# Optimization experiments

Measured on AMD Instinct MI355X. Metric: run time of the kernel, lower is better.

Reference implementation:

```python
import jax, jax.numpy as jnp
import numpy as np

HEADS = 4


def rel_to_abs(x):
    """Convert relative logits [..., L, 2L-1] to absolute [..., L, L].
    out[..., i, j] = x[..., i, j - i + L - 1]."""
    L = x.shape[-2]
    idx = jnp.arange(L)[None, :] - jnp.arange(L)[:, None] + (L - 1)  # [L, L]
    idx = jnp.broadcast_to(idx, x.shape[:-1] + (L,))
    return jnp.take_along_axis(x, idx, axis=-1)


def setup_inputs() -> dict:
    key = jax.random.key(0)
    ks = jax.random.split(key, 5)
    b, c, h, w = 2, 256, 64, 64
    dh = c // HEADS
    return {
        "x": jax.random.normal(ks[0], (b, c, h, w), jnp.float32),
        "w_qkv": jax.random.normal(ks[1], (3 * c, c), jnp.float32) / np.float32(np.sqrt(c)),
        "w_out": jax.random.normal(ks[2], (c, c), jnp.float32) / np.float32(np.sqrt(c)),
        "rel_height": jax.random.normal(ks[3], (2 * h - 1, dh), jnp.float32),
        "rel_width": jax.random.normal(ks[4], (2 * w - 1, dh), jnp.float32),
    }


def reference(x, w_qkv, w_out, rel_height, rel_width):
    b, c, h, w = x.shape
    dh = c // HEADS
    N = h * w
    scale = dh ** -0.5

    # 1x1 conv == per-pixel matmul over channels
    qkv = jnp.einsum('bchw,oc->bohw', x, w_qkv)  # [b, 3c, h, w]
    q, k, v = jnp.split(qkv, 3, axis=1)

    def to_heads(t):  # [b, c, h, w] -> [b, H, N, dh]
        return t.reshape(b, HEADS, dh, N).transpose(0, 1, 3, 2)

    q = to_heads(q) * scale
    k = to_heads(k)
    v = to_heads(v)

    # content-content scores over spatial positions
    content = jnp.einsum('bnid,bnjd->bnij', q, k)  # [b, H, N, N]

    q5 = q.reshape(b, HEADS, h, w, dh)  # [b, H, x, y, dh]
    # width relative logits: [b,H,x,y,2w-1] -> abs -> [b,H,x,y,jw]
    rw = rel_to_abs(jnp.einsum('bnxyd,rd->bnxyr', q5, rel_width))
    # height relative logits on transposed spatial: [b,H,y,x,2h-1] -> [b,H,y,x,jh]
    rh = rel_to_abs(jnp.einsum('bnyxd,rd->bnyxr', q5.transpose(0, 1, 3, 2, 4), rel_height))

    logits = content.reshape(b, HEADS, h, w, h, w)
    logits = logits + rw[:, :, :, :, None, :]  # broadcast width bias over target height jh
    logits = logits + rh.transpose(0, 1, 3, 2, 4)[:, :, :, :, :, None]  # [b,H,x,y,jh] over jw

    attn = jax.nn.softmax(logits.reshape(b, HEADS, N, N), axis=-1)
    out = jnp.einsum('bnij,bnjd->bnid', attn, v)  # [b, H, N, dh]
    out = out.transpose(0, 1, 3, 2).reshape(b, c, h, w)
    out = jnp.einsum('bchw,oc->bohw', out, w_out)  # 1x1 out projection
    return out + x
```

## Files before the change

### kernel.cpp

```cpp
#include <hip/hip_runtime.h>

typedef unsigned short u16;
typedef unsigned int u32;
typedef __bf16 bf16x8 __attribute__((ext_vector_type(8)));
typedef float f32x4 __attribute__((ext_vector_type(4)));
typedef u32 u32x4 __attribute__((ext_vector_type(4)));
typedef u32 u32x2 __attribute__((ext_vector_type(2)));
typedef short s16x4 __attribute__((ext_vector_type(4)));

#define DEVI __device__ __forceinline__

#if defined(__has_builtin)
#if __has_builtin(__builtin_amdgcn_exp2f)
#define EXP2F(x) __builtin_amdgcn_exp2f(x)
#endif
#endif
#ifndef EXP2F
#define EXP2F(x) exp2f(x)
#endif

#define MFMA16(a, b, c) __builtin_amdgcn_mfma_f32_16x16x32_bf16(a, b, c, 0, 0, 0)
#define MFMA1K(a, b, c) __builtin_amdgcn_mfma_f32_16x16x16bf16_1k(a, b, c, 0, 0, 0)

DEVI u16 f2bf(float f) {
    u32 u = __builtin_bit_cast(u32, f);
    u = (u + 0x7FFFu + ((u >> 16) & 1u)) >> 16;
    return (u16)u;
}
DEVI float bf2f(u16 h) {
    u32 u = ((u32)h) << 16;
    return __builtin_bit_cast(float, u);
}
DEVI float bfhi(u32 u) { return __builtin_bit_cast(float, u & 0xFFFF0000u); }
DEVI float bflo(u32 u) { return __builtin_bit_cast(float, u << 16); }
DEVI bf16x8 bc8(u32x4 u) { return __builtin_bit_cast(bf16x8, u); }

#define QSCALE 0.18033688011112042f

__global__ __launch_bounds__(256) void k_prep(const float* __restrict__ x,
                                              const float* __restrict__ wq,
                                              const float* __restrict__ wo,
                                              const float* __restrict__ relh,
                                              const float* __restrict__ relw,
                                              u16* __restrict__ xt, u16* __restrict__ wqb,
                                              u16* __restrict__ wob, u16* __restrict__ relhb,
                                              u16* __restrict__ relwb) {
    int bid = blockIdx.x;
    int t = threadIdx.x;
    if (bid < 512) {
        int pm = bid & 63, cm = (bid >> 6) & 3, b = bid >> 8;
        int p0 = pm * 64, c0 = cm * 64;
        __shared__ float tile[64][65];
#pragma unroll
        for (int it = 0; it < 16; ++it) {
            int idx = it * 256 + t;
            int cl = idx >> 6, pl = idx & 63;
            tile[cl][pl] = x[((size_t)(b * 256 + c0 + cl)) * 4096 + p0 + pl];
        }
        __syncthreads();
#pragma unroll
        for (int it = 0; it < 16; ++it) {
            int idx = it * 256 + t;
            int pl = idx >> 6, cl = idx & 63;
            xt[((size_t)(b * 4096 + p0 + pl)) * 256 + c0 + cl] = f2bf(tile[cl][pl]);
        }
    } else {
        int i0 = (bid - 512) * 256 + t;
#pragma unroll
        for (int i = i0; i < 196608; i += 65536) wqb[i] = f2bf(wq[i]);
        if (i0 < 65536) wob[i0] = f2bf(wo[i0]);
        if (i0 < 8192) {
            relhb[i0] = (i0 < 8128) ? f2bf(relh[i0]) : (u16)0;
            relwb[i0] = (i0 < 8128) ? f2bf(relw[i0]) : (u16)0;
        }
    }
}

__global__ __launch_bounds__(256) void k_qkv(const u16* __restrict__ xt, const u16* __restrict__ wqb,
                                             u16* __restrict__ q, u16* __restrict__ k,
                                             u16* __restrict__ vt) {
    int pm = blockIdx.x, on = blockIdx.y, b = blockIdx.z;
    int p0 = pm * 64, o0 = on * 64;
    __shared__ __align__(16) u16 Bt[64 * 264];
    int t = threadIdx.x;
    int wv = t >> 6, l = t & 63, quad = l >> 4, li = l & 15;

    u32x4 areg[8];
    const u32x4* arow = (const u32x4*)(xt + ((size_t)(b * 4096 + p0 + wv * 16 + li)) * 256);
#pragma unroll
    for (int kc = 0; kc < 8; ++kc) areg[kc] = arow[kc * 4 + quad];

    {
        int row = t >> 2, c0 = (t & 3) * 64;
        const u32x4* g = (const u32x4*)(wqb + (size_t)(o0 + row) * 256 + c0);
        u32x4* s = (u32x4*)(Bt + row * 264 + c0);
#pragma unroll
        for (int kk = 0; kk < 8; ++kk) s[kk] = g[kk];
    }
    __syncthreads();

    f32x4 acc[4] = {{0, 0, 0, 0}, {0, 0, 0, 0}, {0, 0, 0, 0}, {0, 0, 0, 0}};
#pragma unroll
    for (int kc = 0; kc < 8; ++kc) {
        bf16x8 a = bc8(areg[kc]);
#pragma unroll
        for (int ct = 0; ct < 4; ++ct) {
            bf16x8 bb = bc8(*(const u32x4*)(Bt + (ct * 16 + li) * 264 + kc * 32 + quad * 8));
            acc[ct] = MFMA16(a, bb, acc[ct]);
        }
    }

    int tensor = on >> 2, head = on & 3;
    if (tensor == 2) {
        __syncthreads();
        u16* T = Bt;
#pragma unroll
        for (int ct = 0; ct < 4; ++ct)
#pragma unroll
            for (int r = 0; r < 4; ++r)
                T[(ct * 16 + li) * 72 + wv * 16 + quad * 4 + r] = f2bf(acc[ct][r]);
        __syncthreads();
        int dr = t >> 2, pc = (t & 3) * 16;
        u32x4* g = (u32x4*)(vt + ((size_t)((b * 4 + head) * 64 + dr)) * 4096 + p0 + pc);
        const u32x4* s2 = (const u32x4*)(T + dr * 72 + pc);
        g[0] = s2[0];
        g[1] = s2[1];
    } else {
        u16* outp = (tensor == 0) ? q : k;
        float sc = (tensor == 0) ? QSCALE : 1.0f;
#pragma unroll
        for (int ct = 0; ct < 4; ++ct)
#pragma unroll
            for (int r = 0; r < 4; ++r) {
                int p = p0 + wv * 16 + quad * 4 + r;
                int d = ct * 16 + li;
                outp[((size_t)((b * 4 + head) * 4096 + p)) * 64 + d] = f2bf(acc[ct][r] * sc);
            }
    }
}

__global__ __launch_bounds__(256) void k_rel(const u16* __restrict__ q,
                                             const u16* __restrict__ relwb,
                                             const u16* __restrict__ relhb,
                                             u16* __restrict__ Wabs, u16* __restrict__ Habs) {
    int pm = blockIdx.x, bh = blockIdx.y, z = blockIdx.z;
    int p0 = pm * 64;
    const u16* rel = z ? relhb : relwb;
    u16* outp = z ? Habs : Wabs;
    __shared__ __align__(16) u16 Ls[128 * 72];
    int t = threadIdx.x, wv = t >> 6, l = t & 63, quad = l >> 4, li = l & 15;

    {
        int row = t >> 1, half = t & 1;
        const u32x4* g = (const u32x4*)(rel + row * 64 + half * 32);
        u32x4* s = (u32x4*)(Ls + row * 72 + half * 32);
#pragma unroll
        for (int kk = 0; kk < 4; ++kk) s[kk] = g[kk];
    }

    u32x4 aq[2];
    const u32x4* qrow = (const u32x4*)(q + ((size_t)(bh * 4096 + p0 + wv * 16 + li)) * 64);
    aq[0] = qrow[quad];
    aq[1] = qrow[4 + quad];
    __syncthreads();

    f32x4 acc[8];
#pragma unroll
    for (int ct = 0; ct < 8; ++ct) acc[ct] = (f32x4){0.f, 0.f, 0.f, 0.f};
#pragma unroll
    for (int kc = 0; kc < 2; ++kc) {
        bf16x8 a = bc8(aq[kc]);
#pragma unroll
        for (int ct = 0; ct < 8; ++ct) {
            bf16x8 bb = bc8(*(const u32x4*)(Ls + (ct * 16 + li) * 72 + kc * 32 + quad * 8));
            acc[ct] = MFMA16(a, bb, acc[ct]);
        }
    }

#pragma unroll
    for (int ct = 0; ct < 8; ++ct)
#pragma unroll
        for (int r = 0; r < 4; ++r) {
            int row = wv * 16 + quad * 4 + r;
            int p = p0 + row;
            int c = ct * 16 + li;
            int shift = z ? pm : row;
            int j = c - 63 + shift;
            if (j >= 0 && j < 64)
                outp[((size_t)(bh * 4096 + p)) * 64 + j] = f2bf(acc[ct][r]);
        }
}

__global__ __launch_bounds__(256, 2) void k_flash(const u16* __restrict__ q,
                                                  const u16* __restrict__ kg,
                                                  const u16* __restrict__ vt,
                                                  const u16* __restrict__ Wabs,
                                                  const u16* __restrict__ Habs,
                                                  float* __restrict__ OP,
                                                  float* __restrict__ LS) {
    int pm = blockIdx.x, bh = blockIdx.y, ks = blockIdx.z;
    int p0 = pm * 128;
    __shared__ __align__(16) u16 Kt[64 * 72];
    __shared__ __align__(16) u16 Vl[64 * 72];
    __shared__ __align__(16) u16 Hl[128 * 40];
    int t = threadIdx.x, wv = t >> 6, l = t & 63, quad = l >> 4, li = l & 15;
    int rbase = wv * 32;

    u32x4 aq[2][2];
#pragma unroll
    for (int rs = 0; rs < 2; ++rs) {
        const u32x4* qrow =
            (const u32x4*)(q + ((size_t)(bh * 4096 + p0 + rbase + rs * 16 + li)) * 64);
        aq[rs][0] = qrow[quad];
        aq[rs][1] = qrow[4 + quad];
    }

    float wbf[2][4][4];
#pragma unroll
    for (int rs = 0; rs < 2; ++rs)
#pragma unroll
        for (int ct = 0; ct < 4; ++ct) {
            const u32* wp = (const u32*)(Wabs +
                                         ((size_t)(bh * 4096 + p0 + rbase + rs * 16 + li)) * 64 +
                                         ct * 16 + quad * 4);
            u32 lo = wp[0], hi = wp[1];
            wbf[rs][ct][0] = bflo(lo);
            wbf[rs][ct][1] = bfhi(lo);
            wbf[rs][ct][2] = bflo(hi);
            wbf[rs][ct][3] = bfhi(hi);
        }

    {
        int row = t >> 1, ch = (t & 1) * 16;
        const u32x4* g = (const u32x4*)(Habs + ((size_t)(bh * 4096 + p0 + row)) * 64 + ks * 32 + ch);
        u32x4* d = (u32x4*)(Hl + row * 40 + ch);
        d[0] = g[0];
        d[1] = g[1];
    }

    int srow = t >> 2, scc = (t & 3) * 16;
    u32x4 kreg[2], vreg[2];
    {
        int j0 = ks * 2048;
        const u32x4* gk = (const u32x4*)(kg + ((size_t)(bh * 4096 + j0 + srow)) * 64 + scc);
        kreg[0] = gk[0];
        kreg[1] = gk[1];
        const u32x4* gv = (const u32x4*)(vt + ((size_t)(bh * 64 + srow)) * 4096 + j0 + scc);
        vreg[0] = gv[0];
        vreg[1] = gv[1];
    }

    f32x4 oacc[2][5];
#pragma unroll
    for (int rs = 0; rs < 2; ++rs)
#pragma unroll
        for (int ct = 0; ct < 5; ++ct) oacc[rs][ct] = (f32x4){0.f, 0.f, 0.f, 0.f};

    const s16x4 ones = {(short)0x3F80, (short)0x3F80, (short)0x3F80, (short)0x3F80};

    for (int kt = 0; kt < 32; ++kt) {
        {
            u32x4* sk = (u32x4*)(Kt + srow * 72 + scc);
            sk[0] = kreg[0];
            sk[1] = kreg[1];
            u32x4* sv = (u32x4*)(Vl + srow * 72 + scc);
            sv[0] = vreg[0];
            sv[1] = vreg[1];
        }
        __syncthreads();
        if (kt < 31) {
            int j0 = (ks * 32 + kt + 1) * 64;
            const u32x4* gk = (const u32x4*)(kg + ((size_t)(bh * 4096 + j0 + srow)) * 64 + scc);
            kreg[0] = gk[0];
            kreg[1] = gk[1];
            const u32x4* gv = (const u32x4*)(vt + ((size_t)(bh * 64 + srow)) * 4096 + j0 + scc);
            vreg[0] = gv[0];
            vreg[1] = gv[1];
        }

        f32x4 s[2][4];
#pragma unroll
        for (int rs = 0; rs < 2; ++rs)
#pragma unroll
            for (int ct = 0; ct < 4; ++ct) s[rs][ct] = (f32x4){0.f, 0.f, 0.f, 0.f};
#pragma unroll
        for (int kc = 0; kc < 2; ++kc) {
            bf16x8 b0 = bc8(aq[0][kc]), b1 = bc8(aq[1][kc]);
#pragma unroll
            for (int ct = 0; ct < 4; ++ct) {
                bf16x8 af = bc8(*(const u32x4*)(Kt + (ct * 16 + li) * 72 + kc * 32 + quad * 8));
                s[0][ct] = MFMA16(af, b0, s[0][ct]);
                s[1][ct] = MFMA16(af, b1, s[1][ct]);
            }
        }

        s16x4 pf[2][4];
#pragma unroll
        for (int rs = 0; rs < 2; ++rs) {
            float hh = bf2f(Hl[(rbase + rs * 16 + li) * 40 + kt]);
#pragma unroll
            for (int ct = 0; ct < 4; ++ct) {
                u32 e0 = __builtin_bit_cast(u32, EXP2F(s[rs][ct][0] + wbf[rs][ct][0] + hh));
                u32 e1 = __builtin_bit_cast(u32, EXP2F(s[rs][ct][1] + wbf[rs][ct][1] + hh));
                u32 e2 = __builtin_bit_cast(u32, EXP2F(s[rs][ct][2] + wbf[rs][ct][2] + hh));
                u32 e3 = __builtin_bit_cast(u32, EXP2F(s[rs][ct][3] + wbf[rs][ct][3] + hh));
                u32x2 pp;
                pp.x = ((e0 + 0x8000u) >> 16) | ((e1 + 0x8000u) & 0xFFFF0000u);
                pp.y = ((e2 + 0x8000u) >> 16) | ((e3 + 0x8000u) & 0xFFFF0000u);
                pf[rs][ct] = __builtin_bit_cast(s16x4, pp);
            }
        }

#pragma unroll
        for (int jt = 0; jt < 4; ++jt) {
            s16x4 a0 = pf[0][jt], a1 = pf[1][jt];
#pragma unroll
            for (int dt = 0; dt < 4; ++dt) {
                s16x4 bv = __builtin_bit_cast(
                    s16x4, *(const u32x2*)(Vl + (dt * 16 + li) * 72 + jt * 16 + quad * 4));
                oacc[0][dt] = MFMA1K(a0, bv, oacc[0][dt]);
                oacc[1][dt] = MFMA1K(a1, bv, oacc[1][dt]);
            }
            oacc[0][4] = MFMA1K(a0, ones, oacc[0][4]);
            oacc[1][4] = MFMA1K(a1, ones, oacc[1][4]);
        }
        __syncthreads();
    }

#pragma unroll
    for (int rs = 0; rs < 2; ++rs) {
#pragma unroll
        for (int ct = 0; ct < 4; ++ct)
#pragma unroll
            for (int r = 0; r < 4; ++r) {
                int p = p0 + rbase + rs * 16 + quad * 4 + r;
                OP[((size_t)((ks * 8 + bh) * 4096 + p)) * 64 + ct * 16 + li] = oacc[rs][ct][r];
            }
        if (li == 0) {
#pragma unroll
            for (int r = 0; r < 4; ++r) {
                int p = p0 + rbase + rs * 16 + quad * 4 + r;
                LS[(size_t)(ks * 8 + bh) * 4096 + p] = oacc[rs][4][r];
            }
        }
    }
}

__global__ __launch_bounds__(256) void k_out2(const u16* __restrict__ wob,
                                              const float* __restrict__ OP,
                                              const float* __restrict__ LS,
                                              const float* __restrict__ x,
                                              float* __restrict__ out) {
    int pm = blockIdx.x, b = blockIdx.y;
    int p0 = pm * 64;
    __shared__ __align__(16) u16 Bt[64 * 264];
    int t = threadIdx.x, wv = t >> 6, l = t & 63, quad = l >> 4, li = l & 15;

    {
        int row = t >> 2, head = t & 3;
        int bh = b * 4 + head;
        int p = p0 + row;
        const f32x4* o0p = (const f32x4*)(OP + ((size_t)(bh * 4096 + p)) * 64);
        const f32x4* o1p = (const f32x4*)(OP + ((size_t)((8 + bh) * 4096 + p)) * 64);
        float linv = 1.0f / (LS[(size_t)bh * 4096 + p] + LS[(size_t)(8 + bh) * 4096 + p]);
        u16* dst = Bt + row * 264 + head * 64;
#pragma unroll
        for (int kk = 0; kk < 8; ++kk) {
            f32x4 a = o0p[2 * kk], c = o1p[2 * kk];
            f32x4 a2 = o0p[2 * kk + 1], c2 = o1p[2 * kk + 1];
            u32x4 pk;
            u32 u0 = __builtin_bit_cast(u32, (a[0] + c[0]) * linv);
            u32 u1 = __builtin_bit_cast(u32, (a[1] + c[1]) * linv);
            u32 u2 = __builtin_bit_cast(u32, (a[2] + c[2]) * linv);
            u32 u3 = __builtin_bit_cast(u32, (a[3] + c[3]) * linv);
            u32 u4 = __builtin_bit_cast(u32, (a2[0] + c2[0]) * linv);
            u32 u5 = __builtin_bit_cast(u32, (a2[1] + c2[1]) * linv);
            u32 u6 = __builtin_bit_cast(u32, (a2[2] + c2[2]) * linv);
            u32 u7 = __builtin_bit_cast(u32, (a2[3] + c2[3]) * linv);
            pk.x = ((u0 + 0x8000u) >> 16) | ((u1 + 0x8000u) & 0xFFFF0000u);
            pk.y = ((u2 + 0x8000u) >> 16) | ((u3 + 0x8000u) & 0xFFFF0000u);
            pk.z = ((u4 + 0x8000u) >> 16) | ((u5 + 0x8000u) & 0xFFFF0000u);
            pk.w = ((u6 + 0x8000u) >> 16) | ((u7 + 0x8000u) & 0xFFFF0000u);
            *(u32x4*)(dst + kk * 8) = pk;
        }
    }
    __syncthreads();

    for (int com = 0; com < 4; ++com) {
        int co0 = com * 64;
        f32x4 acc[4] = {{0, 0, 0, 0}, {0, 0, 0, 0}, {0, 0, 0, 0}, {0, 0, 0, 0}};
        const u32x4* arow = (const u32x4*)(wob + (size_t)(co0 + wv * 16 + li) * 256);
#pragma unroll
        for (int kc = 0; kc < 8; ++kc) {
            bf16x8 a = bc8(arow[kc * 4 + quad]);
#pragma unroll
            for (int ct = 0; ct < 4; ++ct) {
                bf16x8 bb = bc8(*(const u32x4*)(Bt + (ct * 16 + li) * 264 + kc * 32 + quad * 8));
                acc[ct] = MFMA16(a, bb, acc[ct]);
            }
        }
#pragma unroll
        for (int ct = 0; ct < 4; ++ct)
#pragma unroll
            for (int r = 0; r < 4; ++r) {
                size_t idx =
                    ((size_t)(b * 256 + co0 + wv * 16 + quad * 4 + r)) * 4096 + p0 + ct * 16 + li;
                out[idx] = acc[ct][r] + x[idx];
            }
    }
}

extern "C" void kernel_launch(void* const* d_in, const int* in_sizes, int n_in, void* d_out,
                              int out_size, void* d_ws, size_t ws_size, hipStream_t stream) {
    const float* x = (const float*)d_in[0];
    const float* wqkv = (const float*)d_in[1];
    const float* wout = (const float*)d_in[2];
    const float* relh = (const float*)d_in[3];
    const float* relw = (const float*)d_in[4];
    float* out = (float*)d_out;
    char* ws = (char*)d_ws;

    u16* xt = (u16*)(ws + 0);
    u16* wqb = (u16*)(ws + 4194304);
    u16* wob = (u16*)(ws + 4587520);
    u16* relwb = (u16*)(ws + 4718592);
    u16* relhb = (u16*)(ws + 4734976);
    u16* qb = (u16*)(ws + 4751360);
    u16* kb = (u16*)(ws + 8945664);
    u16* vtb = (u16*)(ws + 13139968);
    u16* Wabs = (u16*)(ws + 17334272);
    u16* Habs = (u16*)(ws + 21528576);
    float* OPart = (float*)(ws + 25722880);
    float* LSum = (float*)(ws + 42500096);

    k_prep<<<768, 256, 0, stream>>>(x, wqkv, wout, relh, relw, xt, wqb, wob, relhb, relwb);
    k_qkv<<<dim3(64, 12, 2), 256, 0, stream>>>(xt, wqb, qb, kb, vtb);
    k_rel<<<dim3(64, 8, 2), 256, 0, stream>>>(qb, relwb, relhb, Wabs, Habs);
    k_flash<<<dim3(32, 8, 2), 256, 0, stream>>>(qb, kb, vtb, Wabs, Habs, OPart, LSum);
    k_out2<<<dim3(64, 2), 256, 0, stream>>>(wob, OPart, LSum, x, out);
}
```

Before: 165.7 us.

## Double-buffer K/V tiles, fold biases into MFMA init, bf16 partials, split out-proj

The flash kernel now double-buffers the K and V shared-memory tiles, which removes one barrier per iteration and lets the next tile's store overlap compute. The width and height bias terms are preloaded into the score accumulator instead of being added after the MFMA. Exponentials are packed with a hardware bf16 convert. The partial attention outputs are stored as bf16 instead of fp32, halving that intermediate traffic, and the output projection grid is split along output channels for more parallelism. The trade-offs are extra shared memory and some precision loss in the partial outputs.

```diff
diff --git a/kernel.cpp b/kernel.cpp
--- a/kernel.cpp
+++ b/kernel.cpp
@@ -3,7 +3,9 @@
 typedef unsigned short u16;
 typedef unsigned int u32;
 typedef __bf16 bf16x8 __attribute__((ext_vector_type(8)));
+typedef __bf16 bf16x2 __attribute__((ext_vector_type(2)));
 typedef float f32x4 __attribute__((ext_vector_type(4)));
+typedef float f32x2 __attribute__((ext_vector_type(2)));
 typedef u32 u32x4 __attribute__((ext_vector_type(4)));
 typedef u32 u32x2 __attribute__((ext_vector_type(2)));
 typedef short s16x4 __attribute__((ext_vector_type(4)));
@@ -34,6 +36,11 @@
 DEVI float bfhi(u32 u) { return __builtin_bit_cast(float, u & 0xFFFF0000u); }
 DEVI float bflo(u32 u) { return __builtin_bit_cast(float, u << 16); }
 DEVI bf16x8 bc8(u32x4 u) { return __builtin_bit_cast(bf16x8, u); }
+DEVI u32 pack2(float a, float b) {
+    f32x2 v = {a, b};
+    bf16x2 h = __builtin_convertvector(v, bf16x2);
+    return __builtin_bit_cast(u32, h);
+}
 
 #define QSCALE 0.18033688011112042f
 
@@ -196,12 +203,12 @@
                                                   const u16* __restrict__ vt,
                                                   const u16* __restrict__ Wabs,
                                                   const u16* __restrict__ Habs,
-                                                  float* __restrict__ OP,
+                                                  u16* __restrict__ OP,
                                                   float* __restrict__ LS) {
     int pm = blockIdx.x, bh = blockIdx.y, ks = blockIdx.z;
     int p0 = pm * 128;
-    __shared__ __align__(16) u16 Kt[64 * 72];
-    __shared__ __align__(16) u16 Vl[64 * 72];
+    __shared__ __align__(16) u16 Kt[2][64 * 72];
+    __shared__ __align__(16) u16 Vl[2][64 * 72];
     __shared__ __align__(16) u16 Hl[128 * 40];
     int t = threadIdx.x, wv = t >> 6, l = t & 63, quad = l >> 4, li = l & 15;
     int rbase = wv * 32;
@@ -215,7 +222,7 @@
         aq[rs][1] = qrow[4 + quad];
     }
 
-    float wbf[2][4][4];
+    f32x4 wb4[2][4];
 #pragma unroll
     for (int rs = 0; rs < 2; ++rs)
 #pragma unroll
@@ -224,10 +231,7 @@
                                          ((size_t)(bh * 4096 + p0 + rbase + rs * 16 + li)) * 64 +
                                          ct * 16 + quad * 4);
             u32 lo = wp[0], hi = wp[1];
-            wbf[rs][ct][0] = bflo(lo);
-            wbf[rs][ct][1] = bfhi(lo);
-            wbf[rs][ct][2] = bflo(hi);
-            wbf[rs][ct][3] = bfhi(hi);
+            wb4[rs][ct] = (f32x4){bflo(lo), bfhi(lo), bflo(hi), bfhi(hi)};
         }
 
     {
@@ -239,15 +243,16 @@
     }
 
     int srow = t >> 2, scc = (t & 3) * 16;
-    u32x4 kreg[2], vreg[2];
     {
         int j0 = ks * 2048;
         const u32x4* gk = (const u32x4*)(kg + ((size_t)(bh * 4096 + j0 + srow)) * 64 + scc);
-        kreg[0] = gk[0];
-        kreg[1] = gk[1];
+        u32x4* sk = (u32x4*)(Kt[0] + srow * 72 + scc);
+        sk[0] = gk[0];
+        sk[1] = gk[1];
         const u32x4* gv = (const u32x4*)(vt + ((size_t)(bh * 64 + srow)) * 4096 + j0 + scc);
-        vreg[0] = gv[0];
-        vreg[1] = gv[1];
+        u32x4* sv = (u32x4*)(Vl[0] + srow * 72 + scc);
+        sv[0] = gv[0];
+        sv[1] = gv[1];
     }
 
     f32x4 oacc[2][5];
@@ -258,16 +263,12 @@
 
     const s16x4 ones = {(short)0x3F80, (short)0x3F80, (short)0x3F80, (short)0x3F80};
 
+    u32x4 kreg[2], vreg[2];
     for (int kt = 0; kt < 32; ++kt) {
-        {
-            u32x4* sk = (u32x4*)(Kt + srow * 72 + scc);
-            sk[0] = kreg[0];
-            sk[1] = kreg[1];
-            u32x4* sv = (u32x4*)(Vl + srow * 72 + scc);
-            sv[0] = vreg[0];
-            sv[1] = vreg[1];
-        }
         __syncthreads();
+        int cur = kt & 1;
+        const u16* Kc = Kt[cur];
+        const u16* Vc = Vl[cur];
         if (kt < 31) {
             int j0 = (ks * 32 + kt + 1) * 64;
             const u32x4* gk = (const u32x4*)(kg + ((size_t)(bh * 4096 + j0 + srow)) * 64 + scc);
@@ -278,17 +279,20 @@
             vreg[1] = gv[1];
         }
 
+        float hh0 = bf2f(Hl[(rbase + li) * 40 + kt]);
+        float hh1 = bf2f(Hl[(rbase + 16 + li) * 40 + kt]);
         f32x4 s[2][4];
 #pragma unroll
-        for (int rs = 0; rs < 2; ++rs)
-#pragma unroll
-            for (int ct = 0; ct < 4; ++ct) s[rs][ct] = (f32x4){0.f, 0.f, 0.f, 0.f};
+        for (int ct = 0; ct < 4; ++ct) {
+            s[0][ct] = wb4[0][ct] + hh0;
+            s[1][ct] = wb4[1][ct] + hh1;
+        }
 #pragma unroll
         for (int kc = 0; kc < 2; ++kc) {
             bf16x8 b0 = bc8(aq[0][kc]), b1 = bc8(aq[1][kc]);
 #pragma unroll
             for (int ct = 0; ct < 4; ++ct) {
-                bf16x8 af = bc8(*(const u32x4*)(Kt + (ct * 16 + li) * 72 + kc * 32 + quad * 8));
+                bf16x8 af = bc8(*(const u32x4*)(Kc + (ct * 16 + li) * 72 + kc * 32 + quad * 8));
                 s[0][ct] = MFMA16(af, b0, s[0][ct]);
                 s[1][ct] = MFMA16(af, b1, s[1][ct]);
             }
@@ -296,20 +300,14 @@
 
         s16x4 pf[2][4];
 #pragma unroll
-        for (int rs = 0; rs < 2; ++rs) {
-            float hh = bf2f(Hl[(rbase + rs * 16 + li) * 40 + kt]);
+        for (int rs = 0; rs < 2; ++rs)
 #pragma unroll
             for (int ct = 0; ct < 4; ++ct) {
-                u32 e0 = __builtin_bit_cast(u32, EXP2F(s[rs][ct][0] + wbf[rs][ct][0] + hh));
-                u32 e1 = __builtin_bit_cast(u32, EXP2F(s[rs][ct][1] + wbf[rs][ct][1] + hh));
-                u32 e2 = __builtin_bit_cast(u32, EXP2F(s[rs][ct][2] + wbf[rs][ct][2] + hh));
-                u32 e3 = __builtin_bit_cast(u32, EXP2F(s[rs][ct][3] + wbf[rs][ct][3] + hh));
                 u32x2 pp;
-                pp.x = ((e0 + 0x8000u) >> 16) | ((e1 + 0x8000u) & 0xFFFF0000u);
-                pp.y = ((e2 + 0x8000u) >> 16) | ((e3 + 0x8000u) & 0xFFFF0000u);
+                pp.x = pack2(EXP2F(s[rs][ct][0]), EXP2F(s[rs][ct][1]));
+                pp.y = pack2(EXP2F(s[rs][ct][2]), EXP2F(s[rs][ct][3]));
                 pf[rs][ct] = __builtin_bit_cast(s16x4, pp);
             }
-        }
 
 #pragma unroll
         for (int jt = 0; jt < 4; ++jt) {
@@ -317,14 +315,22 @@
 #pragma unroll
             for (int dt = 0; dt < 4; ++dt) {
                 s16x4 bv = __builtin_bit_cast(
-                    s16x4, *(const u32x2*)(Vl + (dt * 16 + li) * 72 + jt * 16 + quad * 4));
+                    s16x4, *(const u32x2*)(Vc + (dt * 16 + li) * 72 + jt * 16 + quad * 4));
                 oacc[0][dt] = MFMA1K(a0, bv, oacc[0][dt]);
                 oacc[1][dt] = MFMA1K(a1, bv, oacc[1][dt]);
             }
             oacc[0][4] = MFMA1K(a0, ones, oacc[0][4]);
             oacc[1][4] = MFMA1K(a1, ones, oacc[1][4]);
         }
-        __syncthreads();
+
+        if (kt < 31) {
+            u32x4* sk = (u32x4*)(Kt[cur ^ 1] + srow * 72 + scc);
+            sk[0] = kreg[0];
+            sk[1] = kreg[1];
+            u32x4* sv = (u32x4*)(Vl[cur ^ 1] + srow * 72 + scc);
+            sv[0] = vreg[0];
+            sv[1] = vreg[1];
+        }
     }
 
 #pragma unroll
@@ -334,7 +340,8 @@
 #pragma unroll
             for (int r = 0; r < 4; ++r) {
                 int p = p0 + rbase + rs * 16 + quad * 4 + r;
-                OP[((size_t)((ks * 8 + bh) * 4096 + p)) * 64 + ct * 16 + li] = oacc[rs][ct][r];
+                OP[((size_t)((ks * 8 + bh) * 4096 + p)) * 64 + ct * 16 + li] =
+                    f2bf(oacc[rs][ct][r]);
             }
         if (li == 0) {
 #pragma unroll
@@ -347,11 +354,11 @@
 }
 
 __global__ __launch_bounds__(256) void k_out2(const u16* __restrict__ wob,
-                                              const float* __restrict__ OP,
+                                              const u16* __restrict__ OP,
                                               const float* __restrict__ LS,
                                               const float* __restrict__ x,
                                               float* __restrict__ out) {
-    int pm = blockIdx.x, b = blockIdx.y;
+    int pm = blockIdx.x, b = blockIdx.y, coh = blockIdx.z;
     int p0 = pm * 64;
     __shared__ __align__(16) u16 Bt[64 * 264];
     int t = threadIdx.x, wv = t >> 6, l = t & 63, quad = l >> 4, li = l & 15;
@@ -360,33 +367,26 @@
         int row = t >> 2, head = t & 3;
         int bh = b * 4 + head;
         int p = p0 + row;
-        const f32x4* o0p = (const f32x4*)(OP + ((size_t)(bh * 4096 + p)) * 64);
-        const f32x4* o1p = (const f32x4*)(OP + ((size_t)((8 + bh) * 4096 + p)) * 64);
+        const u32x4* o0p = (const u32x4*)(OP + ((size_t)(bh * 4096 + p)) * 64);
+        const u32x4* o1p = (const u32x4*)(OP + ((size_t)((8 + bh) * 4096 + p)) * 64);
         float linv = 1.0f / (LS[(size_t)bh * 4096 + p] + LS[(size_t)(8 + bh) * 4096 + p]);
         u16* dst = Bt + row * 264 + head * 64;
 #pragma unroll
         for (int kk = 0; kk < 8; ++kk) {
-            f32x4 a = o0p[2 * kk], c = o1p[2 * kk];
-            f32x4 a2 = o0p[2 * kk + 1], c2 = o1p[2 * kk + 1];
+            u32x4 a = o0p[kk], c = o1p[kk];
             u32x4 pk;
-            u32 u0 = __builtin_bit_cast(u32, (a[0] + c[0]) * linv);
-            u32 u1 = __builtin_bit_cast(u32, (a[1] + c[1]) * linv);
-            u32 u2 = __builtin_bit_cast(u32, (a[2] + c[2]) * linv);
-            u32 u3 = __builtin_bit_cast(u32, (a[3] + c[3]) * linv);
-            u32 u4 = __builtin_bit_cast(u32, (a2[0] + c2[0]) * linv);
-            u32 u5 = __builtin_bit_cast(u32, (a2[1] + c2[1]) * linv);
-            u32 u6 = __builtin_bit_cast(u32, (a2[2] + c2[2]) * linv);
-            u32 u7 = __builtin_bit_cast(u32, (a2[3] + c2[3]) * linv);
-            pk.x = ((u0 + 0x8000u) >> 16) | ((u1 + 0x8000u) & 0xFFFF0000u);
-            pk.y = ((u2 + 0x8000u) >> 16) | ((u3 + 0x8000u) & 0xFFFF0000u);
-            pk.z = ((u4 + 0x8000u) >> 16) | ((u5 + 0x8000u) & 0xFFFF0000u);
-            pk.w = ((u6 + 0x8000u) >> 16) | ((u7 + 0x8000u) & 0xFFFF0000u);
+            pk.x = pack2((bflo(a.x) + bflo(c.x)) * linv, (bfhi(a.x) + bfhi(c.x)) * linv);
+            pk.y = pack2((bflo(a.y) + bflo(c.y)) * linv, (bfhi(a.y) + bfhi(c.y)) * linv);
+            pk.z = pack2((bflo(a.z) + bflo(c.z)) * linv, (bfhi(a.z) + bfhi(c.z)) * linv);
+            pk.w = pack2((bflo(a.w) + bflo(c.w)) * linv, (bfhi(a.w) + bfhi(c.w)) * linv);
             *(u32x4*)(dst + kk * 8) = pk;
         }
     }
     __syncthreads();
 
-    for (int com = 0; com < 4; ++com) {
+#pragma unroll
+    for (int ci = 0; ci < 2; ++ci) {
+        int com = coh * 2 + ci;
         int co0 = com * 64;
         f32x4 acc[4] = {{0, 0, 0, 0}, {0, 0, 0, 0}, {0, 0, 0, 0}, {0, 0, 0, 0}};
         const u32x4* arow = (const u32x4*)(wob + (size_t)(co0 + wv * 16 + li) * 256);
@@ -430,12 +430,12 @@
     u16* vtb = (u16*)(ws + 13139968);
     u16* Wabs = (u16*)(ws + 17334272);
     u16* Habs = (u16*)(ws + 21528576);
-    float* OPart = (float*)(ws + 25722880);
-    float* LSum = (float*)(ws + 42500096);
+    u16* OPart = (u16*)(ws + 25722880);
+    float* LSum = (float*)(ws + 34111488);
 
     k_prep<<<768, 256, 0, stream>>>(x, wqkv, wout, relh, relw, xt, wqb, wob, relhb, relwb);
     k_qkv<<<dim3(64, 12, 2), 256, 0, stream>>>(xt, wqb, qb, kb, vtb);
     k_rel<<<dim3(64, 8, 2), 256, 0, stream>>>(qb, relwb, relhb, Wabs, Habs);
     k_flash<<<dim3(32, 8, 2), 256, 0, stream>>>(qb, kb, vtb, Wabs, Habs, OPart, LSum);
-    k_out2<<<dim3(64, 2), 256, 0, stream>>>(wob, OPart, LSum, x, out);
-}
+    k_out2<<<dim3(64, 2, 2), 256, 0, stream>>>(wob, OPart, LSum, x, out);
+}
```

Result: faster. 152.6 us (-7.9%).
